# Performance work log

Measured on AMD Instinct MI355X. Metric: run time of the kernel, lower is better.

The kernel has to match this reference:

```python
import jax, jax.numpy as jnp
import numpy as np

N, B, H, OUT, T = 200000, 1024, 256, 128, 2  # nodes, graphs, hidden(=in_dim), out_dim, timesteps
NEG_SLOPE = 0.01


def setup_inputs() -> dict:
    key = jax.random.key(0)
    ks = jax.random.split(key, 12)
    s = 0.05
    f32 = jnp.float32
    return {
        "x": jax.random.normal(ks[0], (N, H), dtype=f32),
        "batch": jnp.sort(jax.random.randint(ks[1], (N,), 0, B)),
        # GATConv params (heads=1, shared lin for src/dst since in_channels is int)
        "W": jax.random.normal(ks[2], (H, H), dtype=f32) * s,
        "att_src": jax.random.normal(ks[3], (H,), dtype=f32) * s,
        "att_dst": jax.random.normal(ks[4], (H,), dtype=f32) * s,
        "bias_gat": jnp.zeros((H,), dtype=f32),
        # GRUCell params (input_size = H, hidden_size = H)
        "W_ih": jax.random.normal(ks[5], (3 * H, H), dtype=f32) * s,
        "W_hh": jax.random.normal(ks[6], (3 * H, H), dtype=f32) * s,
        "b_ih": jnp.zeros((3 * H,), dtype=f32),
        "b_hh": jnp.zeros((3 * H,), dtype=f32),
        # final Linear
        "W_lin": jax.random.normal(ks[7], (H, OUT), dtype=f32) * s,
        "b_lin": jnp.zeros((OUT,), dtype=f32),
    }


def reference(x, batch, W, att_src, att_dst, bias_gat, W_ih, W_hh, b_ih, b_hh, W_lin, b_lin):
    # out = global_add_pool(x, batch)  -> [B, H]
    out = jax.ops.segment_sum(x, batch, num_segments=B)
    for _ in range(T):
        # --- bipartite GATConv((x, out), edge_index=[arange(N), batch]) ---
        xs = x @ W                       # [N, H] transformed source nodes
        od = out @ W                     # [B, H] transformed dst (graph) nodes
        a_src = xs @ att_src             # [N]
        a_dst = od @ att_dst             # [B]
        e = a_src + a_dst[batch]         # [N] per-edge raw score (one edge per node)
        e = jnp.where(e > 0, e, NEG_SLOPE * e)  # leaky_relu(negative_slope=0.01)
        # scatter-softmax over each graph's incoming edges
        emax = jax.ops.segment_max(e, batch, num_segments=B)
        ee = jnp.exp(e - emax[batch])
        denom = jax.ops.segment_sum(ee, batch, num_segments=B)
        alpha = ee / denom[batch]        # [N]
        # scatter-add aggregation of weighted messages
        agg = jax.ops.segment_sum(xs * alpha[:, None], batch, num_segments=B) + bias_gat
        h = jax.nn.elu(agg)              # [B, H]  (dropout is identity in eval)
        # --- GRUCell(h, out) ---
        gi = h @ W_ih.T + b_ih           # [B, 3H]
        gh = out @ W_hh.T + b_hh         # [B, 3H]
        r = jax.nn.sigmoid(gi[:, :H] + gh[:, :H])
        z = jax.nn.sigmoid(gi[:, H:2 * H] + gh[:, H:2 * H])
        n = jnp.tanh(gi[:, 2 * H:] + r * gh[:, 2 * H:])
        out = jax.nn.silu((1.0 - z) * n + z * out)  # activation = F.silu
    return out @ W_lin + b_lin           # [B, OUT]
```

## Files before the change

### kernel.cpp

```cpp
#include <hip/hip_runtime.h>
#include <math.h>

#define N_NODES 200000
#define BGRAPH  1024
#define HDIM    256
#define ODIM    128
#define CROWS   128
#define SLEN    512

__device__ __forceinline__ unsigned short f2bf(float f) {
    union { float f; unsigned int i; } c; c.f = f;
    unsigned int i = c.i;
    unsigned int r = i + 0x7FFFu + ((i >> 16) & 1u);
    return (unsigned short)(r >> 16);
}
__device__ __forceinline__ float bflo(unsigned int u) {
    union { unsigned int i; float f; } c; c.i = u << 16; return c.f;
}
__device__ __forceinline__ float bfhi(unsigned int u) {
    union { unsigned int i; float f; } c; c.i = u & 0xffff0000u; return c.f;
}

__global__ __launch_bounds__(256) void k_prep(const float* __restrict__ W,
        const float* __restrict__ att_src, const float* __restrict__ att_dst,
        const int* __restrict__ batch, const float* __restrict__ W_ih,
        const float* __restrict__ W_hh, float* __restrict__ v,
        float* __restrict__ u, int* __restrict__ seg,
        unsigned int* __restrict__ Wgu, unsigned int* __restrict__ Wpk) {
    int t = threadIdx.x;
    if (blockIdx.x < 256) {
        int i = blockIdx.x;
        float w = W[(size_t)i * HDIM + t];
        __shared__ float r1[256], r2[256];
        r1[t] = w * att_src[t];
        r2[t] = w * att_dst[t];
        __syncthreads();
        for (int st = 128; st > 0; st >>= 1) {
            if (t < st) { r1[t] += r1[t + st]; r2[t] += r2[t + st]; }
            __syncthreads();
        }
        if (t == 0) { v[i] = r1[0]; u[i] = r2[0]; }
    } else if (blockIdx.x < 261) {
        int b = (blockIdx.x - 256) * 256 + t;
        if (b > BGRAPH) return;
        if (b == BGRAPH) { seg[b] = N_NODES; return; }
        int lo = 0, hi = N_NODES;
        while (lo < hi) { int mid = (lo + hi) >> 1; if (batch[mid] < b) lo = mid + 1; else hi = mid; }
        seg[b] = lo;
    } else if (blockIdx.x < 517) {
        int k = blockIdx.x - 261;
        unsigned int a0 = f2bf(W_ih[(size_t)(0 * HDIM + t) * HDIM + k]);
        unsigned int a1 = f2bf(W_ih[(size_t)(1 * HDIM + t) * HDIM + k]);
        unsigned int a2 = f2bf(W_ih[(size_t)(2 * HDIM + t) * HDIM + k]);
        unsigned int a3 = f2bf(W_hh[(size_t)(0 * HDIM + t) * HDIM + k]);
        unsigned int a4 = f2bf(W_hh[(size_t)(1 * HDIM + t) * HDIM + k]);
        unsigned int a5 = f2bf(W_hh[(size_t)(2 * HDIM + t) * HDIM + k]);
        int kt = k * HDIM + t;
        Wgu[kt]                   = a0 | (a1 << 16);
        Wgu[HDIM * HDIM + kt]     = a2 | (a3 << 16);
        Wgu[2 * HDIM * HDIM + kt] = a4 | (a5 << 16);
    } else {
        int k2 = blockIdx.x - 517;
        unsigned int lo16 = f2bf(W[(size_t)(2 * k2) * HDIM + t]);
        unsigned int hi16 = f2bf(W[(size_t)(2 * k2 + 1) * HDIM + t]);
        Wpk[(size_t)k2 * HDIM + t] = lo16 | (hi16 << 16);
    }
}

__global__ __launch_bounds__(512, 2) void k_fused(const float* __restrict__ x,
        const int* __restrict__ seg, const float* __restrict__ v,
        const float* __restrict__ u, const float* __restrict__ bias_gat,
        const unsigned int* __restrict__ Wgu, const unsigned int* __restrict__ Wpk,
        const float* __restrict__ b_ih, const float* __restrict__ b_hh,
        const float* __restrict__ W_lin, const float* __restrict__ b_lin,
        float* __restrict__ sfall, float* __restrict__ out) {
    int b = blockIdx.x;
    int lo = seg[b], hi = seg[b + 1];
    int len = hi - lo;
    int t = threadIdx.x, wv = t >> 6, lane = t & 63;

    __shared__ unsigned int xc2[CROWS][HDIM / 2];
    __shared__ float s_loc[SLEN];
    __shared__ float comb[8][HDIM];
    __shared__ float red[HDIM];
    __shared__ float axv[HDIM];
    __shared__ float hvec[HDIM];
    __shared__ float oprev[HDIM];
    __shared__ float sred[8], dred[8];

    bool inl = len <= SLEN;
    int clen = len < CROWS ? len : CROWS;
    float ut = u[t & 255];

    float v0 = v[4 * lane + 0], v1 = v[4 * lane + 1];
    float v2 = v[4 * lane + 2], v3 = v[4 * lane + 3];
    float p0 = 0.f, p1 = 0.f, p2 = 0.f, p3 = 0.f;
    float sm = -3.402823466e38f;
    int i = lo + wv;
    for (; i + 8 < hi; i += 16) {
        const float4 r0 = *(const float4*)(x + (size_t)i * HDIM + 4 * lane);
        const float4 r1 = *(const float4*)(x + (size_t)(i + 8) * HDIM + 4 * lane);
        p0 += r0.x + r1.x; p1 += r0.y + r1.y; p2 += r0.z + r1.z; p3 += r0.w + r1.w;
        float pa = r0.x * v0 + r0.y * v1 + r0.z * v2 + r0.w * v3;
        float pb = r1.x * v0 + r1.y * v1 + r1.z * v2 + r1.w * v3;
        #pragma unroll
        for (int off = 32; off > 0; off >>= 1) {
            pa += __shfl_down(pa, off, 64);
            pb += __shfl_down(pb, off, 64);
        }
        int ra = i - lo, rb = ra + 8;
        if (ra < CROWS) {
            unsigned int c0 = (__float_as_uint(r0.y) & 0xffff0000u) | (__float_as_uint(r0.x) >> 16);
            unsigned int c1 = (__float_as_uint(r0.w) & 0xffff0000u) | (__float_as_uint(r0.z) >> 16);
            *(uint2*)&xc2[ra][2 * lane] = make_uint2(c0, c1);
        }
        if (rb < CROWS) {
            unsigned int c0 = (__float_as_uint(r1.y) & 0xffff0000u) | (__float_as_uint(r1.x) >> 16);
            unsigned int c1 = (__float_as_uint(r1.w) & 0xffff0000u) | (__float_as_uint(r1.z) >> 16);
            *(uint2*)&xc2[rb][2 * lane] = make_uint2(c0, c1);
        }
        if (lane == 0) {
            if (inl) { s_loc[ra] = pa; s_loc[rb] = pb; }
            else     { sfall[i] = pa; sfall[i + 8] = pb; }
            sm = fmaxf(sm, fmaxf(pa, pb));
        }
    }
    for (; i < hi; i += 8) {
        const float4 r0 = *(const float4*)(x + (size_t)i * HDIM + 4 * lane);
        p0 += r0.x; p1 += r0.y; p2 += r0.z; p3 += r0.w;
        float pa = r0.x * v0 + r0.y * v1 + r0.z * v2 + r0.w * v3;
        #pragma unroll
        for (int off = 32; off > 0; off >>= 1) pa += __shfl_down(pa, off, 64);
        int ra = i - lo;
        if (ra < CROWS) {
            unsigned int c0 = (__float_as_uint(r0.y) & 0xffff0000u) | (__float_as_uint(r0.x) >> 16);
            unsigned int c1 = (__float_as_uint(r0.w) & 0xffff0000u) | (__float_as_uint(r0.z) >> 16);
            *(uint2*)&xc2[ra][2 * lane] = make_uint2(c0, c1);
        }
        if (lane == 0) {
            if (inl) s_loc[ra] = pa; else sfall[i] = pa;
            sm = fmaxf(sm, pa);
        }
    }
    comb[wv][4 * lane + 0] = p0; comb[wv][4 * lane + 1] = p1;
    comb[wv][4 * lane + 2] = p2; comb[wv][4 * lane + 3] = p3;
    if (lane == 0) sred[wv] = sm;
    __syncthreads();
    if (t < HDIM) {
        float st0 = 0.f;
        #pragma unroll
        for (int j = 0; j < 8; ++j) st0 += comb[j][t];
        oprev[t] = st0;
        red[t] = st0 * ut;
    }
    float smx = fmaxf(fmaxf(fmaxf(sred[0], sred[1]), fmaxf(sred[2], sred[3])),
                      fmaxf(fmaxf(sred[4], sred[5]), fmaxf(sred[6], sred[7])));
    __syncthreads();
    for (int st = 128; st > 0; st >>= 1) { if (t < st) red[t] += red[t + st]; __syncthreads(); }
    float d = red[0];
    __syncthreads();

    int q = t >> 8, tt = t & 255;

    for (int step = 0; step < 2; ++step) {
        float M = smx + d;
        M = M > 0.f ? M : 0.01f * M;

        float a0 = 0.f, a1 = 0.f, a2 = 0.f, a3 = 0.f, den = 0.f;
        int r = wv;
        for (; r + 8 < clen; r += 16) {
            float s0v = inl ? s_loc[r]     : sfall[lo + r];
            float s1v = inl ? s_loc[r + 8] : sfall[lo + r + 8];
            float e0 = s0v + d; e0 = e0 > 0.f ? e0 : 0.01f * e0;
            float e1 = s1v + d; e1 = e1 > 0.f ? e1 : 0.01f * e1;
            float w0 = __expf(e0 - M), w1 = __expf(e1 - M);
            uint2 q0 = *(const uint2*)&xc2[r][2 * lane];
            uint2 q1 = *(const uint2*)&xc2[r + 8][2 * lane];
            den += w0 + w1;
            a0 += w0 * bflo(q0.x) + w1 * bflo(q1.x);
            a1 += w0 * bfhi(q0.x) + w1 * bfhi(q1.x);
            a2 += w0 * bflo(q0.y) + w1 * bflo(q1.y);
            a3 += w0 * bfhi(q0.y) + w1 * bfhi(q1.y);
        }
        for (; r < clen; r += 8) {
            float s0v = inl ? s_loc[r] : sfall[lo + r];
            float e0 = s0v + d; e0 = e0 > 0.f ? e0 : 0.01f * e0;
            float w0 = __expf(e0 - M);
            uint2 q0 = *(const uint2*)&xc2[r][2 * lane];
            den += w0;
            a0 += w0 * bflo(q0.x); a1 += w0 * bfhi(q0.x);
            a2 += w0 * bflo(q0.y); a3 += w0 * bfhi(q0.y);
        }
        for (int rr = clen + wv; rr < len; rr += 8) {
            float sv = inl ? s_loc[rr] : sfall[lo + rr];
            float e0 = sv + d; e0 = e0 > 0.f ? e0 : 0.01f * e0;
            float w0 = __expf(e0 - M);
            const float4 r0 = *(const float4*)(x + (size_t)(lo + rr) * HDIM + 4 * lane);
            den += w0;
            a0 += w0 * r0.x; a1 += w0 * r0.y; a2 += w0 * r0.z; a3 += w0 * r0.w;
        }
        comb[wv][4 * lane + 0] = a0; comb[wv][4 * lane + 1] = a1;
        comb[wv][4 * lane + 2] = a2; comb[wv][4 * lane + 3] = a3;
        if (lane == 0) dred[wv] = den;
        __syncthreads();
        float dtot = (dred[0] + dred[1]) + (dred[2] + dred[3])
                   + (dred[4] + dred[5]) + (dred[6] + dred[7]);
        float inv = (len > 0) ? 1.0f / dtot : 0.f;
        if (t < HDIM) {
            float s8 = 0.f;
            #pragma unroll
            for (int j = 0; j < 8; ++j) s8 += comb[j][t];
            axv[t] = s8 * inv;
        }
        __syncthreads();

        {
            float acc = q ? 0.f : bias_gat[tt];
            int k2e = q * 64 + 64;
            for (int k2 = q * 64; k2 < k2e; ++k2) {
                unsigned int w2 = Wpk[(size_t)k2 * HDIM + tt];
                float2 a2 = *(const float2*)&axv[2 * k2];
                acc += a2.x * bflo(w2) + a2.y * bfhi(w2);
            }
            comb[q][tt] = acc;
        }
        __syncthreads();
        if (t < HDIM) {
            float hs = comb[0][t] + comb[1][t];
            hvec[t] = hs > 0.f ? hs : expm1f(hs);
        }
        __syncthreads();

        float gr = 0.f, gz = 0.f, gn = 0.f, hr = 0.f, hz = 0.f, hn = 0.f;
        {
            int k0e = q * 128 + 128;
            for (int k0 = q * 128; k0 < k0e; k0 += 4) {
                float hq[4], oq[4];
                *(float4*)hq = *(const float4*)&hvec[k0];
                *(float4*)oq = *(const float4*)&oprev[k0];
                #pragma unroll
                for (int j = 0; j < 4; ++j) {
                    int kt = (k0 + j) * HDIM + tt;
                    unsigned int u0 = Wgu[kt];
                    unsigned int u1 = Wgu[HDIM * HDIM + kt];
                    unsigned int u2 = Wgu[2 * HDIM * HDIM + kt];
                    gr += hq[j] * bflo(u0);
                    gz += hq[j] * bfhi(u0);
                    gn += hq[j] * bflo(u1);
                    hr += oq[j] * bfhi(u1);
                    hz += oq[j] * bflo(u2);
                    hn += oq[j] * bfhi(u2);
                }
            }
        }
        if (q == 1) {
            comb[0][tt] = gr; comb[1][tt] = gz; comb[2][tt] = gn;
            comb[3][tt] = hr; comb[4][tt] = hz; comb[5][tt] = hn;
        }
        __syncthreads();
        if (q == 0) {
            float gir = gr + comb[0][tt] + b_ih[tt];
            float giz = gz + comb[1][tt] + b_ih[HDIM + tt];
            float gin = gn + comb[2][tt] + b_ih[2 * HDIM + tt];
            float ghr = hr + comb[3][tt] + b_hh[tt];
            float ghz = hz + comb[4][tt] + b_hh[HDIM + tt];
            float ghn = hn + comb[5][tt] + b_hh[2 * HDIM + tt];
            float rg = 1.f / (1.f + __expf(-(gir + ghr)));
            float zg = 1.f / (1.f + __expf(-(giz + ghz)));
            float ng = tanhf(gin + rg * ghn);
            float prev = oprev[tt];
            float h2 = (1.f - zg) * ng + zg * prev;
            float no = h2 / (1.f + __expf(-h2));
            oprev[tt] = no;
            red[tt] = no * ut;
        }
        __syncthreads();
        for (int st = 128; st > 0; st >>= 1) { if (t < st) red[t] += red[t + st]; __syncthreads(); }
        d = red[0];
        __syncthreads();
    }

    {
        int qq = t >> 7, o = t & 127;
        float acc = 0.f;
        int ke = qq * 64 + 64;
        #pragma unroll 8
        for (int k = qq * 64; k < ke; ++k)
            acc += oprev[k] * W_lin[(size_t)k * ODIM + o];
        comb[qq][o] = acc;
    }
    __syncthreads();
    if (t < ODIM)
        out[(size_t)b * ODIM + t] = (comb[0][t] + comb[1][t])
                                  + (comb[2][t] + comb[3][t]) + b_lin[t];
}

extern "C" void kernel_launch(void* const* d_in, const int* in_sizes, int n_in,
                              void* d_out, int out_size, void* d_ws, size_t ws_size,
                              hipStream_t stream) {
    const float* x        = (const float*)d_in[0];
    const int*   batch    = (const int*)d_in[1];
    const float* W        = (const float*)d_in[2];
    const float* att_src  = (const float*)d_in[3];
    const float* att_dst  = (const float*)d_in[4];
    const float* bias_gat = (const float*)d_in[5];
    const float* W_ih     = (const float*)d_in[6];
    const float* W_hh     = (const float*)d_in[7];
    const float* b_ih     = (const float*)d_in[8];
    const float* b_hh     = (const float*)d_in[9];
    const float* W_lin    = (const float*)d_in[10];
    const float* b_lin    = (const float*)d_in[11];

    char* ws = (char*)d_ws;
    size_t off = 0;
    auto alloc = [&](size_t bytes) {
        void* p = (void*)(ws + off);
        off += (bytes + 255) & ~(size_t)255;
        return p;
    };
    int*          seg   = (int*)alloc((BGRAPH + 1) * 4);
    float*        vv    = (float*)alloc(HDIM * 4);
    float*        uu    = (float*)alloc(HDIM * 4);
    float*        sfall = (float*)alloc((size_t)N_NODES * 4);
    unsigned int* Wgu   = (unsigned int*)alloc((size_t)3 * HDIM * HDIM * 4);
    unsigned int* Wpk   = (unsigned int*)alloc((size_t)(HDIM / 2) * HDIM * 4);

    hipLaunchKernelGGL(k_prep, dim3(645), dim3(256), 0, stream,
                       W, att_src, att_dst, batch, W_ih, W_hh, vv, uu, seg, Wgu, Wpk);
    hipLaunchKernelGGL(k_fused, dim3(BGRAPH), dim3(512), 0, stream,
                       x, seg, vv, uu, bias_gat, Wgu, Wpk, b_ih, b_hh,
                       W_lin, b_lin, sfall, (float*)d_out);
}
```

Baseline: 458.2 us.

## Spill overflow rows as bf16 to workspace, unroll load loop, shuffle-based reductions

Rows beyond the shared-memory cache are now written once as packed bf16 to a global workspace, so each step's tail aggregation reads half the bytes instead of rereading fp32 x. The first-pass load loop is unrolled from two rows to four per wave for more memory-level parallelism. The shared-memory tree reductions for the attention dot product are replaced by wave shuffles plus a four-entry pool, which removes several barriers. In exchange it adds extra global writes for every overflow row and a 100MB workspace, and the tail rows lose precision from bf16 truncation.

```diff
diff --git a/kernel.cpp b/kernel.cpp
--- a/kernel.cpp
+++ b/kernel.cpp
@@ -19,6 +19,9 @@
 }
 __device__ __forceinline__ float bfhi(unsigned int u) {
     union { unsigned int i; float f; } c; c.i = u & 0xffff0000u; return c.f;
+}
+__device__ __forceinline__ unsigned int bfpack(float x, float y) {
+    return (__float_as_uint(y) & 0xffff0000u) | (__float_as_uint(x) >> 16);
 }
 
 __global__ __launch_bounds__(256) void k_prep(const float* __restrict__ W,
@@ -73,7 +76,8 @@
         const unsigned int* __restrict__ Wgu, const unsigned int* __restrict__ Wpk,
         const float* __restrict__ b_ih, const float* __restrict__ b_hh,
         const float* __restrict__ W_lin, const float* __restrict__ b_lin,
-        float* __restrict__ sfall, float* __restrict__ out) {
+        float* __restrict__ sfall, unsigned int* __restrict__ xtb,
+        float* __restrict__ out) {
     int b = blockIdx.x;
     int lo = seg[b], hi = seg[b + 1];
     int len = hi - lo;
@@ -82,11 +86,10 @@
     __shared__ unsigned int xc2[CROWS][HDIM / 2];
     __shared__ float s_loc[SLEN];
     __shared__ float comb[8][HDIM];
-    __shared__ float red[HDIM];
     __shared__ float axv[HDIM];
     __shared__ float hvec[HDIM];
     __shared__ float oprev[HDIM];
-    __shared__ float sred[8], dred[8];
+    __shared__ float sred[8], dred[8], dpool[4];
 
     bool inl = len <= SLEN;
     int clen = len < CROWS ? len : CROWS;
@@ -97,32 +100,51 @@
     float p0 = 0.f, p1 = 0.f, p2 = 0.f, p3 = 0.f;
     float sm = -3.402823466e38f;
     int i = lo + wv;
-    for (; i + 8 < hi; i += 16) {
+    for (; i + 24 < hi; i += 32) {
         const float4 r0 = *(const float4*)(x + (size_t)i * HDIM + 4 * lane);
         const float4 r1 = *(const float4*)(x + (size_t)(i + 8) * HDIM + 4 * lane);
-        p0 += r0.x + r1.x; p1 += r0.y + r1.y; p2 += r0.z + r1.z; p3 += r0.w + r1.w;
+        const float4 r2 = *(const float4*)(x + (size_t)(i + 16) * HDIM + 4 * lane);
+        const float4 r3 = *(const float4*)(x + (size_t)(i + 24) * HDIM + 4 * lane);
+        p0 += (r0.x + r1.x) + (r2.x + r3.x);
+        p1 += (r0.y + r1.y) + (r2.y + r3.y);
+        p2 += (r0.z + r1.z) + (r2.z + r3.z);
+        p3 += (r0.w + r1.w) + (r2.w + r3.w);
         float pa = r0.x * v0 + r0.y * v1 + r0.z * v2 + r0.w * v3;
         float pb = r1.x * v0 + r1.y * v1 + r1.z * v2 + r1.w * v3;
+        float pc = r2.x * v0 + r2.y * v1 + r2.z * v2 + r2.w * v3;
+        float pd = r3.x * v0 + r3.y * v1 + r3.z * v2 + r3.w * v3;
         #pragma unroll
         for (int off = 32; off > 0; off >>= 1) {
             pa += __shfl_down(pa, off, 64);
             pb += __shfl_down(pb, off, 64);
-        }
-        int ra = i - lo, rb = ra + 8;
-        if (ra < CROWS) {
-            unsigned int c0 = (__float_as_uint(r0.y) & 0xffff0000u) | (__float_as_uint(r0.x) >> 16);
-            unsigned int c1 = (__float_as_uint(r0.w) & 0xffff0000u) | (__float_as_uint(r0.z) >> 16);
-            *(uint2*)&xc2[ra][2 * lane] = make_uint2(c0, c1);
-        }
-        if (rb < CROWS) {
-            unsigned int c0 = (__float_as_uint(r1.y) & 0xffff0000u) | (__float_as_uint(r1.x) >> 16);
-            unsigned int c1 = (__float_as_uint(r1.w) & 0xffff0000u) | (__float_as_uint(r1.z) >> 16);
-            *(uint2*)&xc2[rb][2 * lane] = make_uint2(c0, c1);
+            pc += __shfl_down(pc, off, 64);
+            pd += __shfl_down(pd, off, 64);
+        }
+        int ra = i - lo;
+        {
+            unsigned int c0 = bfpack(r0.x, r0.y), c1 = bfpack(r0.z, r0.w);
+            if (ra < CROWS) *(uint2*)&xc2[ra][2 * lane] = make_uint2(c0, c1);
+            else *(uint2*)(xtb + (size_t)i * 128 + 2 * lane) = make_uint2(c0, c1);
+        }
+        {
+            unsigned int c0 = bfpack(r1.x, r1.y), c1 = bfpack(r1.z, r1.w);
+            if (ra + 8 < CROWS) *(uint2*)&xc2[ra + 8][2 * lane] = make_uint2(c0, c1);
+            else *(uint2*)(xtb + (size_t)(i + 8) * 128 + 2 * lane) = make_uint2(c0, c1);
+        }
+        {
+            unsigned int c0 = bfpack(r2.x, r2.y), c1 = bfpack(r2.z, r2.w);
+            if (ra + 16 < CROWS) *(uint2*)&xc2[ra + 16][2 * lane] = make_uint2(c0, c1);
+            else *(uint2*)(xtb + (size_t)(i + 16) * 128 + 2 * lane) = make_uint2(c0, c1);
+        }
+        {
+            unsigned int c0 = bfpack(r3.x, r3.y), c1 = bfpack(r3.z, r3.w);
+            if (ra + 24 < CROWS) *(uint2*)&xc2[ra + 24][2 * lane] = make_uint2(c0, c1);
+            else *(uint2*)(xtb + (size_t)(i + 24) * 128 + 2 * lane) = make_uint2(c0, c1);
         }
         if (lane == 0) {
-            if (inl) { s_loc[ra] = pa; s_loc[rb] = pb; }
-            else     { sfall[i] = pa; sfall[i + 8] = pb; }
-            sm = fmaxf(sm, fmaxf(pa, pb));
+            if (inl) { s_loc[ra] = pa; s_loc[ra + 8] = pb; s_loc[ra + 16] = pc; s_loc[ra + 24] = pd; }
+            else { sfall[i] = pa; sfall[i + 8] = pb; sfall[i + 16] = pc; sfall[i + 24] = pd; }
+            sm = fmaxf(sm, fmaxf(fmaxf(pa, pb), fmaxf(pc, pd)));
         }
     }
     for (; i < hi; i += 8) {
@@ -132,11 +154,9 @@
         #pragma unroll
         for (int off = 32; off > 0; off >>= 1) pa += __shfl_down(pa, off, 64);
         int ra = i - lo;
-        if (ra < CROWS) {
-            unsigned int c0 = (__float_as_uint(r0.y) & 0xffff0000u) | (__float_as_uint(r0.x) >> 16);
-            unsigned int c1 = (__float_as_uint(r0.w) & 0xffff0000u) | (__float_as_uint(r0.z) >> 16);
-            *(uint2*)&xc2[ra][2 * lane] = make_uint2(c0, c1);
-        }
+        unsigned int c0 = bfpack(r0.x, r0.y), c1 = bfpack(r0.z, r0.w);
+        if (ra < CROWS) *(uint2*)&xc2[ra][2 * lane] = make_uint2(c0, c1);
+        else *(uint2*)(xtb + (size_t)i * 128 + 2 * lane) = make_uint2(c0, c1);
         if (lane == 0) {
             if (inl) s_loc[ra] = pa; else sfall[i] = pa;
             sm = fmaxf(sm, pa);
@@ -151,14 +171,15 @@
         #pragma unroll
         for (int j = 0; j < 8; ++j) st0 += comb[j][t];
         oprev[t] = st0;
-        red[t] = st0 * ut;
+        float pr = st0 * ut;
+        #pragma unroll
+        for (int off = 32; off > 0; off >>= 1) pr += __shfl_down(pr, off, 64);
+        if (lane == 0) dpool[wv] = pr;
     }
     float smx = fmaxf(fmaxf(fmaxf(sred[0], sred[1]), fmaxf(sred[2], sred[3])),
                       fmaxf(fmaxf(sred[4], sred[5]), fmaxf(sred[6], sred[7])));
     __syncthreads();
-    for (int st = 128; st > 0; st >>= 1) { if (t < st) red[t] += red[t + st]; __syncthreads(); }
-    float d = red[0];
-    __syncthreads();
+    float d = (dpool[0] + dpool[1]) + (dpool[2] + dpool[3]);
 
     int q = t >> 8, tt = t & 255;
 
@@ -191,13 +212,29 @@
             a0 += w0 * bflo(q0.x); a1 += w0 * bfhi(q0.x);
             a2 += w0 * bflo(q0.y); a3 += w0 * bfhi(q0.y);
         }
-        for (int rr = clen + wv; rr < len; rr += 8) {
+        int rr = clen + wv;
+        for (; rr + 8 < len; rr += 16) {
+            float s0v = inl ? s_loc[rr]     : sfall[lo + rr];
+            float s1v = inl ? s_loc[rr + 8] : sfall[lo + rr + 8];
+            float e0 = s0v + d; e0 = e0 > 0.f ? e0 : 0.01f * e0;
+            float e1 = s1v + d; e1 = e1 > 0.f ? e1 : 0.01f * e1;
+            float w0 = __expf(e0 - M), w1 = __expf(e1 - M);
+            uint2 q0 = *(const uint2*)(xtb + (size_t)(lo + rr) * 128 + 2 * lane);
+            uint2 q1 = *(const uint2*)(xtb + (size_t)(lo + rr + 8) * 128 + 2 * lane);
+            den += w0 + w1;
+            a0 += w0 * bflo(q0.x) + w1 * bflo(q1.x);
+            a1 += w0 * bfhi(q0.x) + w1 * bfhi(q1.x);
+            a2 += w0 * bflo(q0.y) + w1 * bflo(q1.y);
+            a3 += w0 * bfhi(q0.y) + w1 * bfhi(q1.y);
+        }
+        for (; rr < len; rr += 8) {
             float sv = inl ? s_loc[rr] : sfall[lo + rr];
             float e0 = sv + d; e0 = e0 > 0.f ? e0 : 0.01f * e0;
             float w0 = __expf(e0 - M);
-            const float4 r0 = *(const float4*)(x + (size_t)(lo + rr) * HDIM + 4 * lane);
+            uint2 q0 = *(const uint2*)(xtb + (size_t)(lo + rr) * 128 + 2 * lane);
             den += w0;
-            a0 += w0 * r0.x; a1 += w0 * r0.y; a2 += w0 * r0.z; a3 += w0 * r0.w;
+            a0 += w0 * bflo(q0.x); a1 += w0 * bfhi(q0.x);
+            a2 += w0 * bflo(q0.y); a3 += w0 * bfhi(q0.y);
         }
         comb[wv][4 * lane + 0] = a0; comb[wv][4 * lane + 1] = a1;
         comb[wv][4 * lane + 2] = a2; comb[wv][4 * lane + 3] = a3;
@@ -272,12 +309,13 @@
             float h2 = (1.f - zg) * ng + zg * prev;
             float no = h2 / (1.f + __expf(-h2));
             oprev[tt] = no;
-            red[tt] = no * ut;
-        }
-        __syncthreads();
-        for (int st = 128; st > 0; st >>= 1) { if (t < st) red[t] += red[t + st]; __syncthreads(); }
-        d = red[0];
-        __syncthreads();
+            float pr = no * ut;
+            #pragma unroll
+            for (int off = 32; off > 0; off >>= 1) pr += __shfl_down(pr, off, 64);
+            if (lane == 0) dpool[wv] = pr;
+        }
+        __syncthreads();
+        d = (dpool[0] + dpool[1]) + (dpool[2] + dpool[3]);
     }
 
     {
@@ -287,6 +325,7 @@
         #pragma unroll 8
         for (int k = qq * 64; k < ke; ++k)
             acc += oprev[k] * W_lin[(size_t)k * ODIM + o];
+        __syncthreads();
         comb[qq][o] = acc;
     }
     __syncthreads();
@@ -324,10 +363,11 @@
     float*        sfall = (float*)alloc((size_t)N_NODES * 4);
     unsigned int* Wgu   = (unsigned int*)alloc((size_t)3 * HDIM * HDIM * 4);
     unsigned int* Wpk   = (unsigned int*)alloc((size_t)(HDIM / 2) * HDIM * 4);
+    unsigned int* xtb   = (unsigned int*)alloc((size_t)N_NODES * 128 * 4);
 
     hipLaunchKernelGGL(k_prep, dim3(645), dim3(256), 0, stream,
                        W, att_src, att_dst, batch, W_ih, W_hh, vv, uu, seg, Wgu, Wpk);
     hipLaunchKernelGGL(k_fused, dim3(BGRAPH), dim3(512), 0, stream,
                        x, seg, vv, uu, bias_gat, Wgu, Wpk, b_ih, b_hh,
-                       W_lin, b_lin, sfall, (float*)d_out);
-}
+                       W_lin, b_lin, sfall, xtb, (float*)d_out);
+}
```

Measured after the change: 461.8 us. Within noise of the previous version (+0.8%).
